# Kernel tuning notes

Hardware: AMD Instinct MI355X
Metric: run time of the kernel (lower is better)

Reference implementation:

```python
import jax, jax.numpy as jnp
import numpy as np

Q, S, D = 8192, 30, 512
THRESH = 30


def setup_inputs() -> dict:
    key = jax.random.key(0)
    ks = jax.random.split(key, 8)
    return {
        "query_encode": jax.random.normal(ks[0], (Q, D), jnp.float32),
        "support_encode": jax.random.normal(ks[1], (S, D), jnp.float32),
        # binary CTR-style labels in {0,1}
        "support_y": jnp.round(jax.random.uniform(ks[2], (1, S), jnp.float32)),
        "support_predict": jax.random.normal(ks[3], (S,), jnp.float32),
        "query_predict": jax.random.normal(ks[4], (Q,), jnp.float32),
        "fc1_w": jax.random.normal(ks[5], (D,), jnp.float32) / np.sqrt(D),
        "fc1_b": jnp.zeros((), jnp.float32),
        # AdjustLayer params: scale init 6, bias init 0, shape [THRESH, 1]
        "adjust_scale": jnp.full((THRESH, 1), 6.0, jnp.float32),
        "adjust_bias": jnp.zeros((THRESH, 1), jnp.float32),
        "num_samples": S,
    }


def reference(query_encode, support_encode, support_y, support_predict,
              query_predict, fc1_w, fc1_b, adjust_scale, adjust_bias,
              num_samples):
    # Pairwise L1 distance: [Q, S, D]
    distance = jnp.abs(query_encode[:, None, :] - support_encode[None, :, :])
    # Linear scorer over feature dim -> [Q, S]
    similar_score = jnp.einsum("qsd,d->qs", distance, fc1_w) + fc1_b
    attn = jax.nn.softmax(similar_score, axis=1)  # softmax over support dim
    # Residual of support labels vs predictor output: [1, S]
    delta_y = support_y - jax.nn.sigmoid(support_predict)[None, :]
    delta_y_hat = jnp.sum(delta_y * attn, axis=1)  # [Q]
    # AdjustLayer: indexed scale/bias (index is a static int here)
    scale = jnp.abs(adjust_scale[num_samples - 1, 0])
    bias = adjust_bias[num_samples - 1, 0]
    prediction = delta_y_hat * scale + bias + query_predict  # [Q]
    # Mean L2 distance to support set: [Q]
    mean_l2 = jnp.mean(jnp.sqrt(jnp.sum(distance ** 2, axis=-1)), axis=-1)
    return prediction, mean_l2
```

## Files before the change

### kernel.cpp

```cpp
#include <hip/hip_runtime.h>
#include <math.h>


#define QN 8192
#define SN 30
#define DN 512
#define BLK 256
#define QT 16
#define SROW 572
#define SCHUNK 15
#define PSTR 31

__global__ __launch_bounds__(BLK, 2)
void resus_one(const float* __restrict__ query,
               const float* __restrict__ support,
               const float* __restrict__ support_y,
               const float* __restrict__ support_pr,
               const float* __restrict__ query_pr,
               const float* __restrict__ fc1_w,
               const float* __restrict__ adj_scale,
               const float* __restrict__ adj_bias,
               const int*   __restrict__ num_samples,
               float* __restrict__ out)
{
    __shared__ float  sp[SCHUNK * SROW];
    __shared__ float2 part[4 * QT * PSTR];

    const int tid  = threadIdx.x;
    const int ql   = tid & 15;
    const int dseg = tid >> 4;
    const int wv   = tid >> 6;
    const int dloc = dseg & 3;
    const int q    = blockIdx.x * QT + ql;

    const float* qp = query + (size_t)q * DN + dseg * 32;
    float4 q0 = *reinterpret_cast<const float4*>(qp +  0);
    float4 q1 = *reinterpret_cast<const float4*>(qp +  4);
    float4 q2 = *reinterpret_cast<const float4*>(qp +  8);
    float4 q3 = *reinterpret_cast<const float4*>(qp + 12);
    float4 q4 = *reinterpret_cast<const float4*>(qp + 16);
    float4 q5 = *reinterpret_cast<const float4*>(qp + 20);
    float4 q6 = *reinterpret_cast<const float4*>(qp + 24);
    float4 q7 = *reinterpret_cast<const float4*>(qp + 28);
    const float* wp = fc1_w + dseg * 32;
    float4 w0 = *reinterpret_cast<const float4*>(wp +  0);
    float4 w1 = *reinterpret_cast<const float4*>(wp +  4);
    float4 w2 = *reinterpret_cast<const float4*>(wp +  8);
    float4 w3 = *reinterpret_cast<const float4*>(wp + 12);
    float4 w4 = *reinterpret_cast<const float4*>(wp + 16);
    float4 w5 = *reinterpret_cast<const float4*>(wp + 20);
    float4 w6 = *reinterpret_cast<const float4*>(wp + 24);
    float4 w7 = *reinterpret_cast<const float4*>(wp + 28);

#define PIN4(V) asm volatile("" : "+v"((V).x), "+v"((V).y), "+v"((V).z), "+v"((V).w))
    PIN4(q0); PIN4(q1); PIN4(q2); PIN4(q3);
    PIN4(q4); PIN4(q5); PIN4(q6); PIN4(q7);
    PIN4(w0); PIN4(w1); PIN4(w2); PIN4(w3);
    PIN4(w4); PIN4(w5); PIN4(w6); PIN4(w7);
#undef PIN4

#define ACC4(QV, WV, SV) { float d_; \
    d_ = (QV).x - (SV).x; sc = fmaf((WV).x, fabsf(d_), sc); sq = fmaf(d_, d_, sq); \
    d_ = (QV).y - (SV).y; sc = fmaf((WV).y, fabsf(d_), sc); sq = fmaf(d_, d_, sq); \
    d_ = (QV).z - (SV).z; sc = fmaf((WV).z, fabsf(d_), sc); sq = fmaf(d_, d_, sq); \
    d_ = (QV).w - (SV).w; sc = fmaf((WV).w, fabsf(d_), sc); sq = fmaf(d_, d_, sq); }

    const int sbase = dseg * 36;

    for (int pass = 0; pass < 2; ++pass) {
        __syncthreads();

        const float4* sg = reinterpret_cast<const float4*>(
            support + (size_t)pass * SCHUNK * DN);
        for (int i = tid; i < SCHUNK * 128; i += BLK) {
            const int row = i >> 7, c4 = i & 127;
            *reinterpret_cast<float4*>(
                sp + row * SROW + 36 * (c4 >> 3) + 4 * (c4 & 7)) = sg[i];
        }
        __syncthreads();

#pragma unroll 5
        for (int sl = 0; sl < SCHUNK; ++sl) {
            const float* sr = sp + sl * SROW + sbase;
            const float4 s0 = *reinterpret_cast<const float4*>(sr +  0);
            const float4 s1 = *reinterpret_cast<const float4*>(sr +  4);
            const float4 s2 = *reinterpret_cast<const float4*>(sr +  8);
            const float4 s3 = *reinterpret_cast<const float4*>(sr + 12);
            const float4 s4 = *reinterpret_cast<const float4*>(sr + 16);
            const float4 s5 = *reinterpret_cast<const float4*>(sr + 20);
            const float4 s6 = *reinterpret_cast<const float4*>(sr + 24);
            const float4 s7 = *reinterpret_cast<const float4*>(sr + 28);

            float sc = 0.0f, sq = 0.0f;
            ACC4(q0, w0, s0) ACC4(q1, w1, s1)
            ACC4(q2, w2, s2) ACC4(q3, w3, s3)
            ACC4(q4, w4, s4) ACC4(q5, w5, s5)
            ACC4(q6, w6, s6) ACC4(q7, w7, s7)

            sc += __shfl_xor(sc, 16); sq += __shfl_xor(sq, 16);
            sc += __shfl_xor(sc, 32); sq += __shfl_xor(sq, 32);

            if (dloc == 0) {
                const int sg_ = pass * SCHUNK + sl;
                part[(wv * QT + ql) * PSTR + sg_] = make_float2(sc, sq);
            }
        }
    }
#undef ACC4
    __syncthreads();

    const int grp  = tid >> 5;
    const int s32  = tid & 31;
    const bool valid = (s32 < SN);
    const int  si  = valid ? s32 : 0;

    float dy = 0.0f;
    if (valid)
        dy = support_y[s32] - 1.0f / (1.0f + expf(-support_pr[s32]));

    const int ns = num_samples[0];
    const float ascale = fabsf(adj_scale[ns - 1]);
    const float abias  = adj_bias[ns - 1];

#pragma unroll
    for (int it = 0; it < 2; ++it) {
        const int qloc = grp + 8 * it;
        const int qg   = blockIdx.x * QT + qloc;

        const float2 p0 = part[(0 * QT + qloc) * PSTR + si];
        const float2 p1 = part[(1 * QT + qloc) * PSTR + si];
        const float2 p2 = part[(2 * QT + qloc) * PSTR + si];
        const float2 p3 = part[(3 * QT + qloc) * PSTR + si];
        float scv = ((p0.x + p1.x) + p2.x) + p3.x;
        float ssv = ((p0.y + p1.y) + p2.y) + p3.y;

        if (!valid) { scv = -1e30f; ssv = 0.0f; }

        float m = scv;
#pragma unroll
        for (int off = 16; off >= 1; off >>= 1)
            m = fmaxf(m, __shfl_xor(m, off));

        float e   = valid ? expf(scv - m) : 0.0f;
        float den = e;
        float num = dy * e;
        float l2  = valid ? sqrtf(ssv) : 0.0f;
#pragma unroll
        for (int off = 16; off >= 1; off >>= 1) {
            den += __shfl_xor(den, off);
            num += __shfl_xor(num, off);
            l2  += __shfl_xor(l2,  off);
        }

        if (s32 == 0) {
            out[qg]      = num / den * ascale + abias + query_pr[qg];
            out[QN + qg] = l2 * (1.0f / (float)SN);
        }
    }
}

extern "C" void kernel_launch(void* const* d_in, const int* in_sizes, int n_in,
                              void* d_out, int out_size, void* d_ws, size_t ws_size,
                              hipStream_t stream)
{
    const float* query      = (const float*)d_in[0];
    const float* support    = (const float*)d_in[1];
    const float* support_y  = (const float*)d_in[2];
    const float* support_pr = (const float*)d_in[3];
    const float* query_pr   = (const float*)d_in[4];
    const float* fc1_w      = (const float*)d_in[5];
    const float* adj_scale  = (const float*)d_in[7];
    const float* adj_bias   = (const float*)d_in[8];
    const int*   num_s      = (const int*)d_in[9];
    float* out = (float*)d_out;

    dim3 grid(QN / QT);
    hipLaunchKernelGGL(resus_one, grid, dim3(BLK), 0, stream,
                       query, support, support_y, support_pr, query_pr,
                       fc1_w, adj_scale, adj_bias, num_s, out);
}
```

Measured before the change: 100.6 us.

## Replace cross-lane shuffle reduction with shared-memory partials and raise occupancy

```diff
diff --git a/kernel.cpp b/kernel.cpp
--- a/kernel.cpp
+++ b/kernel.cpp
@@ -7,11 +7,15 @@
 #define DN 512
 #define BLK 256
 #define QT 16
+#define SCHUNK 10
+#define NPASS 3
 #define SROW 572
-#define SCHUNK 15
+#undef SROW
+#define SROW 580
+#define PRW 17
 #define PSTR 31
 
-__global__ __launch_bounds__(BLK, 2)
+__global__ __launch_bounds__(BLK, 3)
 void resus_one(const float* __restrict__ query,
                const float* __restrict__ support,
                const float* __restrict__ support_y,
@@ -24,13 +28,12 @@
                float* __restrict__ out)
 {
     __shared__ float  sp[SCHUNK * SROW];
-    __shared__ float2 part[4 * QT * PSTR];
+    __shared__ float2 praw[SCHUNK * QT * PRW];
+    __shared__ float2 part[QT * PSTR];
 
     const int tid  = threadIdx.x;
     const int ql   = tid & 15;
     const int dseg = tid >> 4;
-    const int wv   = tid >> 6;
-    const int dloc = dseg & 3;
     const int q    = blockIdx.x * QT + ql;
 
     const float* qp = query + (size_t)q * DN + dseg * 32;
@@ -67,7 +70,7 @@
 
     const int sbase = dseg * 36;
 
-    for (int pass = 0; pass < 2; ++pass) {
+    for (int pass = 0; pass < NPASS; ++pass) {
         __syncthreads();
 
         const float4* sg = reinterpret_cast<const float4*>(
@@ -97,13 +100,17 @@
             ACC4(q4, w4, s4) ACC4(q5, w5, s5)
             ACC4(q6, w6, s6) ACC4(q7, w7, s7)
 
-            sc += __shfl_xor(sc, 16); sq += __shfl_xor(sq, 16);
-            sc += __shfl_xor(sc, 32); sq += __shfl_xor(sq, 32);
+            praw[(sl * QT + ql) * PRW + dseg] = make_float2(sc, sq);
+        }
+        __syncthreads();
 
-            if (dloc == 0) {
-                const int sg_ = pass * SCHUNK + sl;
-                part[(wv * QT + ql) * PSTR + sg_] = make_float2(sc, sq);
-            }
+        if (tid < SCHUNK * QT) {
+            const int sl = tid >> 4, qq = tid & 15;
+            const float2* r = &praw[(sl * QT + qq) * PRW];
+            float sc = 0.0f, sq = 0.0f;
+#pragma unroll
+            for (int d = 0; d < 16; ++d) { sc += r[d].x; sq += r[d].y; }
+            part[qq * PSTR + pass * SCHUNK + sl] = make_float2(sc, sq);
         }
     }
 #undef ACC4
@@ -126,15 +133,10 @@
     for (int it = 0; it < 2; ++it) {
         const int qloc = grp + 8 * it;
         const int qg   = blockIdx.x * QT + qloc;
+        const float2 pr = part[qloc * PSTR + si];
 
-        const float2 p0 = part[(0 * QT + qloc) * PSTR + si];
-        const float2 p1 = part[(1 * QT + qloc) * PSTR + si];
-        const float2 p2 = part[(2 * QT + qloc) * PSTR + si];
-        const float2 p3 = part[(3 * QT + qloc) * PSTR + si];
-        float scv = ((p0.x + p1.x) + p2.x) + p3.x;
-        float ssv = ((p0.y + p1.y) + p2.y) + p3.y;
-
-        if (!valid) { scv = -1e30f; ssv = 0.0f; }
+        float scv = valid ? pr.x : -1e30f;
+        float ssv = valid ? pr.y : 0.0f;
 
         float m = scv;
 #pragma unroll
```

After: 190.5 us. 1.89x slower.
